# Performance work log

Hardware: AMD Instinct MI355X
Metric: run time of the kernel (lower is better)

The kernel has to match this reference:

```python
import jax, jax.numpy as jnp
import numpy as np

N_LEVELS = 16
F = 2
LOG2_T = 19
T = 1 << LOG2_T
BASE_RES = 16.0
FINEST_RES = 512.0
N_SAMPLES = 128
NEAR, FAR = 2.0, 6.0
BOX_MIN = jnp.array([-1.5, -1.5, -1.5], jnp.float32)
BOX_MAX = jnp.array([1.5, 1.5, 1.5], jnp.float32)
GEO_FEAT = 15
OUT_CH = 4

_PRIMES = np.array([1, 2654435761, 805459861], dtype=np.uint32)
_OFFSETS = np.array([[i, j, k] for i in (0, 1) for j in (0, 1) for k in (0, 1)], dtype=np.int32)  # [8,3]
_B = np.exp((np.log(FINEST_RES) - np.log(BASE_RES)) / (N_LEVELS - 1))
_RESOLUTIONS = np.floor(BASE_RES * _B ** np.arange(N_LEVELS)).astype(np.float32)


def setup_inputs() -> dict:
    key = jax.random.key(0)
    ks = jax.random.split(key, 10)
    n_rays = 16384
    o = jax.random.uniform(ks[0], (n_rays, 3), jnp.float32, -0.5, 0.5)
    d = jax.random.normal(ks[1], (n_rays, 3), jnp.float32)
    d = d / jnp.linalg.norm(d, axis=-1, keepdims=True)
    rays = jnp.concatenate([o, d], -1)
    hash_tables = jax.random.uniform(ks[2], (N_LEVELS, T, F), jnp.float32, -1e-4, 1e-4)
    def w(k, di, do):
        return jax.random.normal(k, (di, do), jnp.float32) * (1.0 / np.sqrt(di))
    return dict(
        rays=rays,
        hash_tables=hash_tables,
        ws0=w(ks[3], 32, 64), ws1=w(ks[4], 64, 64), ws2=w(ks[5], 64, 1 + GEO_FEAT),
        wc0=w(ks[6], 16 + GEO_FEAT, 64), wc1=w(ks[7], 64, 64), wc2=w(ks[8], 64, 64), wc3=w(ks[9], 64, OUT_CH - 1),
    )


def _hash_embed(x, tables):
    """Multi-res hash grid: x [P,3] world coords, tables [L,T,F] -> ([P,L*F], keep_mask [P])."""
    xc = jnp.clip(x, BOX_MIN, BOX_MAX)
    keep = jnp.all(x == xc, axis=-1)
    offs = jnp.asarray(_OFFSETS)          # [8,3]
    primes = jnp.asarray(_PRIMES)         # uint32
    feats = []
    for l in range(N_LEVELS):
        grid = (BOX_MAX - BOX_MIN) / _RESOLUTIONS[l]
        bl = jnp.floor((xc - BOX_MIN) / grid).astype(jnp.int32)   # [P,3] bottom-left voxel index
        vmin = bl.astype(jnp.float32) * grid + BOX_MIN
        wts = (xc - vmin) / grid                                  # trilinear weights [P,3]
        corners = (bl[:, None, :] + offs[None]).astype(jnp.uint32)  # [P,8,3]
        h = (corners[..., 0] * primes[0]) ^ (corners[..., 1] * primes[1]) ^ (corners[..., 2] * primes[2])
        idx = (h & jnp.uint32(T - 1)).astype(jnp.int32)           # [P,8]
        e = tables[l][idx]                                        # [P,8,F]
        w0, w1, w2 = wts[:, 0:1], wts[:, 1:2], wts[:, 2:3]
        c00 = e[:, 0] * (1 - w0) + e[:, 4] * w0
        c01 = e[:, 1] * (1 - w0) + e[:, 5] * w0
        c10 = e[:, 2] * (1 - w0) + e[:, 6] * w0
        c11 = e[:, 3] * (1 - w0) + e[:, 7] * w0
        c0 = c00 * (1 - w1) + c10 * w1
        c1 = c01 * (1 - w1) + c11 * w1
        feats.append(c0 * (1 - w2) + c1 * w2)
    return jnp.concatenate(feats, -1), keep


def _sh_encode(d):
    """Degree-4 spherical harmonics encoding, [P,3] -> [P,16]."""
    x, y, z = d[..., 0], d[..., 1], d[..., 2]
    xx, yy, zz = x * x, y * y, z * z
    xy, yz, xz = x * y, y * z, x * z
    C0 = 0.28209479177387814
    C1 = 0.4886025119029199
    C2 = (1.0925484305920792, -1.0925484305920792, 0.31539156525252005, -1.0925484305920792, 0.5462742152960396)
    C3 = (-0.5900435899266435, 2.890611442640554, -0.4570457994644658, 0.3731763325901154,
          -0.4570457994644658, 1.445305721320277, -0.5900435899266435)
    return jnp.stack([
        jnp.full_like(x, C0),
        -C1 * y, C1 * z, -C1 * x,
        C2[0] * xy, C2[1] * yz, C2[2] * (2.0 * zz - xx - yy), C2[3] * xz, C2[4] * (xx - yy),
        C3[0] * y * (3.0 * xx - yy), C3[1] * xy * z, C3[2] * y * (4.0 * zz - xx - yy),
        C3[3] * z * (2.0 * zz - 3.0 * xx - 3.0 * yy), C3[4] * x * (4.0 * zz - xx - yy),
        C3[5] * z * (xx - yy), C3[6] * x * (xx - 3.0 * yy),
    ], axis=-1)


def _forward(rays, hash_tables, ws0, ws1, ws2, wc0, wc1, wc2, wc3):
    n_rays = rays.shape[0]
    o, d = rays[:, :3], rays[:, 3:6]
    z = jnp.linspace(NEAR, FAR, N_SAMPLES, dtype=jnp.float32)
    zvals = jnp.broadcast_to(z, (n_rays, N_SAMPLES))
    pts = o[:, None, :] + d[:, None, :] * z[None, :, None]       # [N,S,3]
    P = n_rays * N_SAMPLES
    pts_f = pts.reshape(P, 3)
    dirs_f = jnp.broadcast_to(d[:, None, :], (n_rays, N_SAMPLES, 3)).reshape(P, 3)

    enc_pts, keep = _hash_embed(pts_f, hash_tables)              # [P,32], [P]
    enc_dirs = _sh_encode(dirs_f)                                # [P,16]

    # NeRFSmall: bias-free sigma net then color net
    h = jnp.maximum(enc_pts @ ws0, 0.0)
    h = jnp.maximum(h @ ws1, 0.0)
    h = h @ ws2                                                   # [P, 1+GEO_FEAT]
    sigma, geo = h[:, 0], h[:, 1:]
    hc = jnp.concatenate([enc_dirs, geo], -1)
    hc = jnp.maximum(hc @ wc0, 0.0)
    hc = jnp.maximum(hc @ wc1, 0.0)
    hc = jnp.maximum(hc @ wc2, 0.0)
    color = hc @ wc3                                              # [P, OUT_CH-1]

    sigma = jnp.where(keep, sigma, 0.0)                           # output[~keep_mask, -1] = 0
    raw = jnp.concatenate([color, sigma[:, None]], -1).reshape(n_rays, N_SAMPLES, OUT_CH)

    # Integrator (raw2outputs)
    dists = zvals[:, 1:] - zvals[:, :-1]
    dists = jnp.concatenate([dists, jnp.full((n_rays, 1), 1e10, jnp.float32)], -1)
    dists = dists * jnp.linalg.norm(d, axis=-1, keepdims=True)
    chs = jax.nn.sigmoid(raw[..., :-1])
    alpha = 1.0 - jnp.exp(-jnp.maximum(raw[..., -1], 0.0) * dists)
    trans = jnp.cumprod(1.0 - alpha + 1e-10, axis=-1)
    trans = jnp.concatenate([jnp.ones((n_rays, 1), jnp.float32), trans[:, :-1]], -1)
    weights = alpha * trans
    chs_map = jnp.einsum('ns,nsc->nc', weights, chs)
    depth_map = jnp.sum(weights * zvals, -1)
    probs = jnp.concatenate([weights, 1.0 - jnp.sum(weights, -1, keepdims=True) + 1e-6], -1)
    p = probs / jnp.sum(probs, -1, keepdims=True)
    sparsity_loss = -jnp.sum(p * jnp.log(jnp.clip(p, 1e-37)), -1)
    return chs_map, depth_map, sparsity_loss


def reference(rays, hash_tables, ws0, ws1, ws2, wc0, wc1, wc2, wc3):
    return _forward(rays, hash_tables, ws0, ws1, ws2, wc0, wc1, wc2, wc3)
```

## Files before the change

### kernel.cpp

```cpp
#include <hip/hip_runtime.h>

#define NRAYS 16384
#define NLEV  16
#define THASH 524288
#define MAXACT 48
#define MAXPTS (NRAYS*MAXACT)
#define MBLK  512
#define MGRID 1024

__device__ __forceinline__ float zval32(int i) {
  const float step = 4.0f / 127.0f;
  return __fadd_rn(2.0f, __fmul_rn((float)i, step));
}
__device__ __forceinline__ float pcoord(float o, float d, float z) {
  return __fadd_rn(o, __fmul_rn(d, z));
}

__global__ __launch_bounds__(64)
void k_classify(const float* __restrict__ rays,
                float* __restrict__ sh,
                unsigned* __restrict__ rn) {
  int r = blockIdx.x * 64 + threadIdx.x;
  if (r >= NRAYS) return;
  float ox = rays[6*r+0], oy = rays[6*r+1], oz = rays[6*r+2];
  float dx = rays[6*r+3], dy = rays[6*r+4], dz = rays[6*r+5];
  float x = dx, y = dy, z = dz;
  float xx = x*x, yy = y*y, zz = z*z, xy = x*y, yz = y*z, xz = x*z;
  float* shp = sh + 16*r;
  shp[0]  = 0.28209479177387814f;
  shp[1]  = -0.4886025119029199f * y;
  shp[2]  =  0.4886025119029199f * z;
  shp[3]  = -0.4886025119029199f * x;
  shp[4]  =  1.0925484305920792f * xy;
  shp[5]  = -1.0925484305920792f * yz;
  shp[6]  =  0.31539156525252005f * (2.0f*zz - xx - yy);
  shp[7]  = -1.0925484305920792f * xz;
  shp[8]  =  0.5462742152960396f * (xx - yy);
  shp[9]  = -0.5900435899266435f * y * (3.0f*xx - yy);
  shp[10] =  2.890611442640554f  * xy * z;
  shp[11] = -0.4570457994644658f * y * (4.0f*zz - xx - yy);
  shp[12] =  0.3731763325901154f * z * (2.0f*zz - 3.0f*xx - 3.0f*yy);
  shp[13] = -0.4570457994644658f * x * (4.0f*zz - xx - yy);
  shp[14] =  1.445305721320277f  * z * (xx - yy);
  shp[15] = -0.5900435899266435f * x * (xx - 3.0f*yy);
  int n = 0;
  for (int i = 0; i < 128; ++i) {
    float zi = zval32(i);
    float px = pcoord(ox, dx, zi);
    float py = pcoord(oy, dy, zi);
    float pz = pcoord(oz, dz, zi);
    bool in = (px >= -1.5f) && (px <= 1.5f) && (py >= -1.5f) && (py <= 1.5f)
           && (pz >= -1.5f) && (pz <= 1.5f);
    if (!in) break;
    ++n;
  }
  rn[r] = (unsigned)n;
}

__global__ __launch_bounds__(1024)
void k_scan(const unsigned* __restrict__ rn,
            unsigned* __restrict__ rbase,
            unsigned* __restrict__ counter,
            unsigned* __restrict__ plist) {
  __shared__ unsigned wsum[16];
  const int t = threadIdx.x;
  const int lane = t & 63, wid = t >> 6;
  unsigned nv[16];
  const uint4* rn4 = (const uint4*)rn;
  unsigned tot = 0;
#pragma unroll
  for (int k = 0; k < 4; ++k) {
    uint4 a = rn4[t*4 + k];
    nv[4*k+0] = a.x; nv[4*k+1] = a.y; nv[4*k+2] = a.z; nv[4*k+3] = a.w;
    tot += a.x + a.y + a.z + a.w;
  }
  unsigned incl = tot;
#pragma unroll
  for (int off = 1; off < 64; off <<= 1) {
    unsigned v = __shfl_up(incl, off);
    if (lane >= off) incl += v;
  }
  if (lane == 63) wsum[wid] = incl;
  __syncthreads();
  if (t == 0) {
    unsigned acc = 0;
#pragma unroll
    for (int w = 0; w < 16; ++w) { unsigned x = wsum[w]; wsum[w] = acc; acc += x; }
    *counter = acc;
  }
  __syncthreads();
  unsigned base = wsum[wid] + (incl - tot);
#pragma unroll
  for (int j = 0; j < 16; ++j) {
    int r = t*16 + j;
    rbase[r] = base;
    unsigned nj = nv[j];
    for (unsigned i = 0; i < nj; ++i) plist[base + i] = (unsigned)(r*128) + i;
    base += nj;
  }
}

template<int IN, int TOTOUT, int JC, bool RELU>
__device__ __forceinline__ void layer(const float* __restrict__ W, int jbase,
                                      const float* __restrict__ in,
                                      float* __restrict__ out, int lane) {
  float acc[JC];
#pragma unroll
  for (int j = 0; j < JC; ++j) acc[j] = 0.0f;
#pragma unroll 8
  for (int k = 0; k < IN; ++k) {
    float a = in[k*64 + lane];
    const float* Wk = W + k*TOTOUT + jbase;
#pragma unroll
    for (int j = 0; j < JC; ++j) acc[j] = fmaf(a, Wk[j], acc[j]);
  }
#pragma unroll
  for (int j = 0; j < JC; ++j)
    out[(jbase + j)*64 + lane] = RELU ? fmaxf(acc[j], 0.0f) : acc[j];
}

__global__ __launch_bounds__(MBLK)
void k_mlp(const float* __restrict__ rays,
           const float* __restrict__ tables,
           const float* __restrict__ w_s0, const float* __restrict__ w_s1,
           const float* __restrict__ w_s2, const float* __restrict__ w_c0,
           const float* __restrict__ w_c1, const float* __restrict__ w_c2,
           const float* __restrict__ w_c3,
           const float* __restrict__ sh,
           const unsigned* __restrict__ counter,
           const unsigned* __restrict__ plist,
           float4* __restrict__ results) {
  __shared__ float bufA[64*64];
  __shared__ float bufB[64*64];
  __shared__ float sig_s[64];
  __shared__ unsigned pid_s[64];
  const int t = threadIdx.x;
  const int lane = t & 63;
  const int q = __builtin_amdgcn_readfirstlane(t >> 6);
  {
    float pf = 0.f;
    const float4* a;
    a = (const float4*)w_s0; for (int i = t; i < 512;  i += MBLK) pf += a[i].x;
    a = (const float4*)w_s1; for (int i = t; i < 1024; i += MBLK) pf += a[i].x;
    a = (const float4*)w_s2; for (int i = t; i < 256;  i += MBLK) pf += a[i].x;
    a = (const float4*)w_c0; for (int i = t; i < 496;  i += MBLK) pf += a[i].x;
    a = (const float4*)w_c1; for (int i = t; i < 1024; i += MBLK) pf += a[i].x;
    a = (const float4*)w_c2; for (int i = t; i < 1024; i += MBLK) pf += a[i].x;
    a = (const float4*)w_c3; for (int i = t; i < 48;   i += MBLK) pf += a[i].x;
    asm volatile("" :: "v"(pf));
  }
  const unsigned count = *counter;
  const unsigned ntiles = (count + 63u) >> 6;
  const float RESF[NLEV] = {16.f,20.f,25.f,32.f,40.f,50.f,64.f,80.f,
                            101.f,128.f,161.f,203.f,256.f,322.f,406.f,512.f};
  for (unsigned tile = blockIdx.x; tile < ntiles; tile += MGRID) {
    unsigned s0 = tile << 6;
    if (t < 64) {
      unsigned s = s0 + (unsigned)t;
      pid_s[t] = (s < count) ? plist[s] : 0u;
    }
    __syncthreads();
    {
      unsigned pid = pid_s[lane];
      int r = (int)(pid >> 7);
      int i = (int)(pid & 127u);
      float zi = zval32(i);
      float px = pcoord(rays[6*r+0], rays[6*r+3], zi);
      float py = pcoord(rays[6*r+1], rays[6*r+4], zi);
      float pz = pcoord(rays[6*r+2], rays[6*r+5], zi);
      float xcx = fminf(fmaxf(px, -1.5f), 1.5f);
      float xcy = fminf(fmaxf(py, -1.5f), 1.5f);
      float xcz = fminf(fmaxf(pz, -1.5f), 1.5f);
#pragma unroll
      for (int li = 0; li < 2; ++li) {
        int l = 2*q + li;
        const float grid = 3.0f / RESF[l];
        float bfx = floorf(__fdiv_rn(__fadd_rn(xcx, 1.5f), grid));
        float bfy = floorf(__fdiv_rn(__fadd_rn(xcy, 1.5f), grid));
        float bfz = floorf(__fdiv_rn(__fadd_rn(xcz, 1.5f), grid));
        float vmx = __fadd_rn(__fmul_rn(bfx, grid), -1.5f);
        float vmy = __fadd_rn(__fmul_rn(bfy, grid), -1.5f);
        float vmz = __fadd_rn(__fmul_rn(bfz, grid), -1.5f);
        float wx = __fdiv_rn(__fsub_rn(xcx, vmx), grid);
        float wy = __fdiv_rn(__fsub_rn(xcy, vmy), grid);
        float wz = __fdiv_rn(__fsub_rn(xcz, vmz), grid);
        unsigned cx0 = (unsigned)(int)bfx, cy0 = (unsigned)(int)bfy, cz0 = (unsigned)(int)bfz;
        unsigned cx1 = cx0 + 1u, cy1 = cy0 + 1u, cz1 = cz0 + 1u;
        unsigned hy0 = cy0*2654435761u, hy1 = cy1*2654435761u;
        unsigned hz0 = cz0*805459861u,  hz1 = cz1*805459861u;
        const float2* tb = (const float2*)tables + (size_t)l*THASH;
        float2 e000 = tb[(cx0^hy0^hz0)&(THASH-1)];
        float2 e001 = tb[(cx0^hy0^hz1)&(THASH-1)];
        float2 e010 = tb[(cx0^hy1^hz0)&(THASH-1)];
        float2 e011 = tb[(cx0^hy1^hz1)&(THASH-1)];
        float2 e100 = tb[(cx1^hy0^hz0)&(THASH-1)];
        float2 e101 = tb[(cx1^hy0^hz1)&(THASH-1)];
        float2 e110 = tb[(cx1^hy1^hz0)&(THASH-1)];
        float2 e111 = tb[(cx1^hy1^hz1)&(THASH-1)];
        float iwx = 1.f-wx, iwy = 1.f-wy, iwz = 1.f-wz;
        float c00a = e000.x*iwx + e100.x*wx, c00b = e000.y*iwx + e100.y*wx;
        float c01a = e001.x*iwx + e101.x*wx, c01b = e001.y*iwx + e101.y*wx;
        float c10a = e010.x*iwx + e110.x*wx, c10b = e010.y*iwx + e110.y*wx;
        float c11a = e011.x*iwx + e111.x*wx, c11b = e011.y*iwx + e111.y*wx;
        float c0a = c00a*iwy + c10a*wy, c0b = c00b*iwy + c10b*wy;
        float c1a = c01a*iwy + c11a*wy, c1b = c01b*iwy + c11b*wy;
        bufA[(2*l+0)*64 + lane] = c0a*iwz + c1a*wz;
        bufA[(2*l+1)*64 + lane] = c0b*iwz + c1b*wz;
      }
    }
    __syncthreads();
    layer<32,64,8,true >(w_s0, q*8, bufA, bufB, lane); __syncthreads();
    layer<64,64,8,true >(w_s1, q*8, bufB, bufA, lane); __syncthreads();
    layer<64,16,2,false>(w_s2, q*2, bufA, bufB, lane); __syncthreads();
    if (q == 0) sig_s[lane] = bufB[0*64 + lane];
    for (int idx = t; idx < 31*64; idx += MBLK) {
      int k = idx >> 6, p = idx & 63;
      float v;
      if (k < 16) v = sh[(pid_s[p] >> 7)*16 + k];
      else        v = bufB[(k-15)*64 + p];
      bufA[idx] = v;
    }
    __syncthreads();
    layer<31,64,8,true >(w_c0, q*8, bufA, bufB, lane); __syncthreads();
    layer<64,64,8,true >(w_c1, q*8, bufB, bufA, lane); __syncthreads();
    layer<64,64,8,true >(w_c2, q*8, bufA, bufB, lane); __syncthreads();
    if (q < 3) layer<64,3,1,false>(w_c3, q, bufB, bufA, lane);
    __syncthreads();
    if (q == 0) {
      unsigned s = s0 + (unsigned)lane;
      if (s < count) {
        float4 res;
        res.x = sig_s[lane];
        res.y = bufA[0*64 + lane];
        res.z = bufA[1*64 + lane];
        res.w = bufA[2*64 + lane];
        results[s] = res;
      }
    }
    __syncthreads();
  }
}

__global__ __launch_bounds__(64)
void k_comp(const float* __restrict__ rays,
            const unsigned* __restrict__ rbase,
            const unsigned* __restrict__ rn,
            const float4* __restrict__ results,
            float* __restrict__ out) {
  int r = blockIdx.x * 64 + threadIdx.x;
  if (r >= NRAYS) return;
  float dx = rays[6*r+3], dy = rays[6*r+4], dz = rays[6*r+5];
  float dnorm = sqrtf(dx*dx + dy*dy + dz*dz);
  int n = (int)rn[r];
  unsigned base = rbase[r];
  const float step = 4.0f/127.0f;
  const float diststep = __fmul_rn(step, dnorm);
  float S = 0.f, ch0 = 0.f, ch1 = 0.f, ch2 = 0.f, dep = 0.f, trans = 1.f;
  for (int i = 0; i < n; ++i) {
    float4 rs = results[base + i];
    float z = zval32(i);
    float sg = fmaxf(rs.x, 0.f);
    float alpha = -expm1f(-__fmul_rn(sg, diststep));
    float w = __fmul_rn(alpha, trans);
    trans = __fmul_rn(trans, __fadd_rn(__fsub_rn(1.f, alpha), 1e-10f));
    float s0 = 1.f/(1.f + expf(-rs.y));
    float s1 = 1.f/(1.f + expf(-rs.z));
    float s2 = 1.f/(1.f + expf(-rs.w));
    S += w; ch0 += w*s0; ch1 += w*s1; ch2 += w*s2; dep += w*z;
  }
  float rem  = __fadd_rn(__fsub_rn(1.f, S), 1e-6f);
  float Stot = __fadd_rn(S, rem);
  float loss = 0.f, trans2 = 1.f;
  for (int i = 0; i < n; ++i) {
    float4 rs = results[base + i];
    float sg = fmaxf(rs.x, 0.f);
    float alpha = -expm1f(-__fmul_rn(sg, diststep));
    float w = __fmul_rn(alpha, trans2);
    trans2 = __fmul_rn(trans2, __fadd_rn(__fsub_rn(1.f, alpha), 1e-10f));
    float p = __fdiv_rn(w, Stot);
    loss += p * logf(fmaxf(p, 1e-37f));
  }
  float pl = __fdiv_rn(rem, Stot);
  loss += pl * logf(fmaxf(pl, 1e-37f));
  out[3*r+0] = ch0; out[3*r+1] = ch1; out[3*r+2] = ch2;
  out[3*NRAYS + r] = dep;
  out[4*NRAYS + r] = -loss;
}

extern "C" void kernel_launch(void* const* d_in, const int* in_sizes, int n_in,
                              void* d_out, int out_size, void* d_ws, size_t ws_size,
                              hipStream_t stream) {
  const float* rays   = (const float*)d_in[0];
  const float* tables = (const float*)d_in[1];
  const float* ws0    = (const float*)d_in[2];
  const float* ws1    = (const float*)d_in[3];
  const float* ws2    = (const float*)d_in[4];
  const float* wc0    = (const float*)d_in[5];
  const float* wc1    = (const float*)d_in[6];
  const float* wc2    = (const float*)d_in[7];
  const float* wc3    = (const float*)d_in[8];

  char* ws = (char*)d_ws;
  unsigned* counter = (unsigned*)ws;
  unsigned* rbase   = (unsigned*)(ws + 256);
  unsigned* rn      = (unsigned*)(ws + 256 + 65536);
  float*    sh      = (float*)  (ws + 256 + 131072);
  float4*   results = (float4*) (ws + 1179904);
  unsigned* plist   = (unsigned*)(ws + 1179904 + (size_t)MAXPTS*16);

  k_classify<<<NRAYS/64, 64, 0, stream>>>(rays, sh, rn);
  k_scan<<<1, 1024, 0, stream>>>(rn, rbase, counter, plist);
  k_mlp<<<MGRID, MBLK, 0, stream>>>(rays, tables, ws0, ws1, ws2,
                                    wc0, wc1, wc2, wc3, sh, counter, plist, results);
  k_comp<<<NRAYS/64, 64, 0, stream>>>(rays, rbase, rn, results, (float*)d_out);
}
```

Baseline: 216.0 us.

## Stage all MLP weights in LDS and run two tiles per 1024-thread block

The fused MLP kernel now copies every network weight into dynamic shared memory once per block and reads them from LDS with vectorized float4/float2 loads, instead of reading weights from global memory in every layer. Blocks grow to 1024 threads, each handling two 64-point tiles in parallel, on a persistent grid of 256 blocks. This is meant to cut repeated global/L2 weight traffic. In exchange the block needs about 137 KB of LDS, which limits occupancy to one block per CU, and block-wide barriers now couple the two tile groups.

New measurement: 254.3 us. +17.8%, slower.

```diff
diff --git a/kernel.cpp b/kernel.cpp
--- a/kernel.cpp
+++ b/kernel.cpp
@@ -5,8 +5,22 @@
 #define THASH 524288
 #define MAXACT 48
 #define MAXPTS (NRAYS*MAXACT)
-#define MBLK  512
-#define MGRID 1024
+#define MBLK2 1024
+#define MGRID2 256
+
+#define OFF_S0 0
+#define OFF_S1 2048
+#define OFF_S2 6144
+#define OFF_C0 7168
+#define OFF_C1 9152
+#define OFF_C2 13248
+#define OFF_C3 17344
+#define OFF_BUFA 17536
+#define OFF_BUFB 25728
+#define OFF_SIG  33920
+#define OFF_PID  34048
+#define SMEM_FLOATS 34176
+#define SMEM_BYTES  (SMEM_FLOATS*4)
 
 __device__ __forceinline__ float zval32(int i) {
   const float step = 4.0f / 127.0f;
@@ -100,26 +114,46 @@
   }
 }
 
+extern __shared__ float smem[];
+
 template<int IN, int TOTOUT, int JC, bool RELU>
-__device__ __forceinline__ void layer(const float* __restrict__ W, int jbase,
-                                      const float* __restrict__ in,
-                                      float* __restrict__ out, int lane) {
+__device__ __forceinline__ void layer_lds(const float* Wl, int jbase,
+                                          const float* in, float* out, int lane) {
   float acc[JC];
 #pragma unroll
   for (int j = 0; j < JC; ++j) acc[j] = 0.0f;
-#pragma unroll 8
-  for (int k = 0; k < IN; ++k) {
-    float a = in[k*64 + lane];
-    const float* Wk = W + k*TOTOUT + jbase;
-#pragma unroll
-    for (int j = 0; j < JC; ++j) acc[j] = fmaf(a, Wk[j], acc[j]);
+  if constexpr (JC == 8) {
+#pragma unroll 4
+    for (int k = 0; k < IN; ++k) {
+      float a = in[k*64 + lane];
+      const float4* w4 = (const float4*)(Wl + k*TOTOUT + jbase);
+      float4 wa = w4[0], wb = w4[1];
+      acc[0] = fmaf(a, wa.x, acc[0]); acc[1] = fmaf(a, wa.y, acc[1]);
+      acc[2] = fmaf(a, wa.z, acc[2]); acc[3] = fmaf(a, wa.w, acc[3]);
+      acc[4] = fmaf(a, wb.x, acc[4]); acc[5] = fmaf(a, wb.y, acc[5]);
+      acc[6] = fmaf(a, wb.z, acc[6]); acc[7] = fmaf(a, wb.w, acc[7]);
+    }
+  } else if constexpr (JC == 2) {
+#pragma unroll 4
+    for (int k = 0; k < IN; ++k) {
+      float a = in[k*64 + lane];
+      float2 w = *(const float2*)(Wl + k*TOTOUT + jbase);
+      acc[0] = fmaf(a, w.x, acc[0]); acc[1] = fmaf(a, w.y, acc[1]);
+    }
+  } else {
+#pragma unroll 4
+    for (int k = 0; k < IN; ++k) {
+      float a = in[k*64 + lane];
+#pragma unroll
+      for (int j = 0; j < JC; ++j) acc[j] = fmaf(a, Wl[k*TOTOUT + jbase + j], acc[j]);
+    }
   }
 #pragma unroll
   for (int j = 0; j < JC; ++j)
     out[(jbase + j)*64 + lane] = RELU ? fmaxf(acc[j], 0.0f) : acc[j];
 }
 
-__global__ __launch_bounds__(MBLK)
+__global__ __launch_bounds__(MBLK2)
 void k_mlp(const float* __restrict__ rays,
            const float* __restrict__ tables,
            const float* __restrict__ w_s0, const float* __restrict__ w_s1,
@@ -130,37 +164,43 @@
            const unsigned* __restrict__ counter,
            const unsigned* __restrict__ plist,
            float4* __restrict__ results) {
-  __shared__ float bufA[64*64];
-  __shared__ float bufB[64*64];
-  __shared__ float sig_s[64];
-  __shared__ unsigned pid_s[64];
   const int t = threadIdx.x;
+  {
+    float4* d = (float4*)smem;
+    const float4* s;
+    s = (const float4*)w_s0; for (int i = t; i < 512;  i += MBLK2) d[i]        = s[i];
+    s = (const float4*)w_s1; for (int i = t; i < 1024; i += MBLK2) d[512+i]    = s[i];
+    s = (const float4*)w_s2; for (int i = t; i < 256;  i += MBLK2) d[1536+i]   = s[i];
+    s = (const float4*)w_c0; for (int i = t; i < 496;  i += MBLK2) d[1792+i]   = s[i];
+    s = (const float4*)w_c1; for (int i = t; i < 1024; i += MBLK2) d[2288+i]   = s[i];
+    s = (const float4*)w_c2; for (int i = t; i < 1024; i += MBLK2) d[3312+i]   = s[i];
+    s = (const float4*)w_c3; for (int i = t; i < 48;   i += MBLK2) d[4336+i]   = s[i];
+  }
+  const int g    = t >> 9;
+  const int tg   = t & 511;
   const int lane = t & 63;
-  const int q = __builtin_amdgcn_readfirstlane(t >> 6);
-  {
-    float pf = 0.f;
-    const float4* a;
-    a = (const float4*)w_s0; for (int i = t; i < 512;  i += MBLK) pf += a[i].x;
-    a = (const float4*)w_s1; for (int i = t; i < 1024; i += MBLK) pf += a[i].x;
-    a = (const float4*)w_s2; for (int i = t; i < 256;  i += MBLK) pf += a[i].x;
-    a = (const float4*)w_c0; for (int i = t; i < 496;  i += MBLK) pf += a[i].x;
-    a = (const float4*)w_c1; for (int i = t; i < 1024; i += MBLK) pf += a[i].x;
-    a = (const float4*)w_c2; for (int i = t; i < 1024; i += MBLK) pf += a[i].x;
-    a = (const float4*)w_c3; for (int i = t; i < 48;   i += MBLK) pf += a[i].x;
-    asm volatile("" :: "v"(pf));
-  }
-  const unsigned count = *counter;
+  const int q    = __builtin_amdgcn_readfirstlane((t >> 6) & 7);
+  float*    Wl     = smem;
+  float*    bufA   = smem + OFF_BUFA + (g << 12);
+  float*    bufB   = smem + OFF_BUFB + (g << 12);
+  float*    sig_s  = smem + OFF_SIG  + g*64;
+  unsigned* pid_s  = (unsigned*)(smem + OFF_PID) + g*64;
+  __syncthreads();
+  const unsigned count  = *counter;
   const unsigned ntiles = (count + 63u) >> 6;
+  const unsigned rounds = (ntiles + 511u) >> 9;
   const float RESF[NLEV] = {16.f,20.f,25.f,32.f,40.f,50.f,64.f,80.f,
                             101.f,128.f,161.f,203.f,256.f,322.f,406.f,512.f};
-  for (unsigned tile = blockIdx.x; tile < ntiles; tile += MGRID) {
-    unsigned s0 = tile << 6;
-    if (t < 64) {
-      unsigned s = s0 + (unsigned)t;
-      pid_s[t] = (s < count) ? plist[s] : 0u;
-    }
-    __syncthreads();
-    {
+  for (unsigned rd = 0; rd < rounds; ++rd) {
+    const unsigned tile = rd*512u + (unsigned)blockIdx.x*2u + (unsigned)g;
+    const bool active = (tile < ntiles);
+    const unsigned s0 = tile << 6;
+    if (active && tg < 64) {
+      unsigned s = s0 + (unsigned)tg;
+      pid_s[tg] = (s < count) ? plist[s] : 0u;
+    }
+    __syncthreads();
+    if (active) {
       unsigned pid = pid_s[lane];
       int r = (int)(pid >> 7);
       int i = (int)(pid & 127u);
@@ -209,24 +249,32 @@
       }
     }
     __syncthreads();
-    layer<32,64,8,true >(w_s0, q*8, bufA, bufB, lane); __syncthreads();
-    layer<64,64,8,true >(w_s1, q*8, bufB, bufA, lane); __syncthreads();
-    layer<64,16,2,false>(w_s2, q*2, bufA, bufB, lane); __syncthreads();
-    if (q == 0) sig_s[lane] = bufB[0*64 + lane];
-    for (int idx = t; idx < 31*64; idx += MBLK) {
-      int k = idx >> 6, p = idx & 63;
-      float v;
-      if (k < 16) v = sh[(pid_s[p] >> 7)*16 + k];
-      else        v = bufB[(k-15)*64 + p];
-      bufA[idx] = v;
-    }
-    __syncthreads();
-    layer<31,64,8,true >(w_c0, q*8, bufA, bufB, lane); __syncthreads();
-    layer<64,64,8,true >(w_c1, q*8, bufB, bufA, lane); __syncthreads();
-    layer<64,64,8,true >(w_c2, q*8, bufA, bufB, lane); __syncthreads();
-    if (q < 3) layer<64,3,1,false>(w_c3, q, bufB, bufA, lane);
-    __syncthreads();
-    if (q == 0) {
+    if (active) layer_lds<32,64,8,true >(Wl+OFF_S0, q*8, bufA, bufB, lane);
+    __syncthreads();
+    if (active) layer_lds<64,64,8,true >(Wl+OFF_S1, q*8, bufB, bufA, lane);
+    __syncthreads();
+    if (active) layer_lds<64,16,2,false>(Wl+OFF_S2, q*2, bufA, bufB, lane);
+    __syncthreads();
+    if (active) {
+      if (q == 0) sig_s[lane] = bufB[0*64 + lane];
+      for (int idx = tg; idx < 31*64; idx += 512) {
+        int k = idx >> 6, p = idx & 63;
+        float v;
+        if (k < 16) v = sh[(pid_s[p] >> 7)*16 + k];
+        else        v = bufB[(k-15)*64 + p];
+        bufA[idx] = v;
+      }
+    }
+    __syncthreads();
+    if (active) layer_lds<31,64,8,true >(Wl+OFF_C0, q*8, bufA, bufB, lane);
+    __syncthreads();
+    if (active) layer_lds<64,64,8,true >(Wl+OFF_C1, q*8, bufB, bufA, lane);
+    __syncthreads();
+    if (active) layer_lds<64,64,8,true >(Wl+OFF_C2, q*8, bufA, bufB, lane);
+    __syncthreads();
+    if (active && q < 3) layer_lds<64,3,1,false>(Wl+OFF_C3, q, bufB, bufA, lane);
+    __syncthreads();
+    if (active && q == 0) {
       unsigned s = s0 + (unsigned)lane;
       if (s < count) {
         float4 res;
@@ -290,6 +338,12 @@
 extern "C" void kernel_launch(void* const* d_in, const int* in_sizes, int n_in,
                               void* d_out, int out_size, void* d_ws, size_t ws_size,
                               hipStream_t stream) {
+  static int smem_set = 0;
+  if (!smem_set) {
+    hipFuncSetAttribute((const void*)k_mlp,
+                        hipFuncAttributeMaxDynamicSharedMemorySize, SMEM_BYTES);
+    smem_set = 1;
+  }
   const float* rays   = (const float*)d_in[0];
   const float* tables = (const float*)d_in[1];
   const float* ws0    = (const float*)d_in[2];
@@ -310,7 +364,8 @@
 
   k_classify<<<NRAYS/64, 64, 0, stream>>>(rays, sh, rn);
   k_scan<<<1, 1024, 0, stream>>>(rn, rbase, counter, plist);
-  k_mlp<<<MGRID, MBLK, 0, stream>>>(rays, tables, ws0, ws1, ws2,
-                                    wc0, wc1, wc2, wc3, sh, counter, plist, results);
+  k_mlp<<<MGRID2, MBLK2, SMEM_BYTES, stream>>>(rays, tables, ws0, ws1, ws2,
+                                               wc0, wc1, wc2, wc3, sh, counter,
+                                               plist, results);
   k_comp<<<NRAYS/64, 64, 0, stream>>>(rays, rbase, rn, results, (float*)d_out);
 }
```

## Fuse classify, scan, MLP and compositing into one cooperative persistent kernel

Applied to the files above, without the earlier changes.

Replaces the four separate launches with a single cooperative kernel of 768 blocks of 512 threads, using grid-wide syncs between the classify, scan, MLP and compositing phases. The aim is to remove launch gaps and per-kernel ramp-up and drain between stages. The scan is still done by one block, and the MLP loop now strides by 768 blocks instead of 1024. The weight-prefetch warmup loop is dropped. The old four-kernel path stays as a fallback if the cooperative launch fails. Risks are the cost of each grid.sync, 768 blocks possibly not all being co-resident (which makes the cooperative launch fail), and the light classify and compositing phases using few threads per block.

Measured after the change: 468.7 us. 2.17x slower.

```diff
diff --git a/kernel.cpp b/kernel.cpp
--- a/kernel.cpp
+++ b/kernel.cpp
@@ -1,10 +1,14 @@
 #include <hip/hip_runtime.h>
+#include <hip/hip_cooperative_groups.h>
+
+namespace cg = cooperative_groups;
 
 #define NRAYS 16384
 #define NLEV  16
 #define THASH 524288
 #define MAXACT 48
 #define MAXPTS (NRAYS*MAXACT)
+#define FGRID 768
 #define MBLK  512
 #define MGRID 1024
 
@@ -16,12 +20,9 @@
   return __fadd_rn(o, __fmul_rn(d, z));
 }
 
-__global__ __launch_bounds__(64)
-void k_classify(const float* __restrict__ rays,
-                float* __restrict__ sh,
-                unsigned* __restrict__ rn) {
-  int r = blockIdx.x * 64 + threadIdx.x;
-  if (r >= NRAYS) return;
+__device__ __forceinline__ void classify_body(const float* __restrict__ rays,
+                                              float* __restrict__ sh,
+                                              unsigned* __restrict__ rn, int r) {
   float ox = rays[6*r+0], oy = rays[6*r+1], oz = rays[6*r+2];
   float dx = rays[6*r+3], dy = rays[6*r+4], dz = rays[6*r+5];
   float x = dx, y = dy, z = dz;
@@ -57,198 +58,11 @@
   rn[r] = (unsigned)n;
 }
 
-__global__ __launch_bounds__(1024)
-void k_scan(const unsigned* __restrict__ rn,
-            unsigned* __restrict__ rbase,
-            unsigned* __restrict__ counter,
-            unsigned* __restrict__ plist) {
-  __shared__ unsigned wsum[16];
-  const int t = threadIdx.x;
-  const int lane = t & 63, wid = t >> 6;
-  unsigned nv[16];
-  const uint4* rn4 = (const uint4*)rn;
-  unsigned tot = 0;
-#pragma unroll
-  for (int k = 0; k < 4; ++k) {
-    uint4 a = rn4[t*4 + k];
-    nv[4*k+0] = a.x; nv[4*k+1] = a.y; nv[4*k+2] = a.z; nv[4*k+3] = a.w;
-    tot += a.x + a.y + a.z + a.w;
-  }
-  unsigned incl = tot;
-#pragma unroll
-  for (int off = 1; off < 64; off <<= 1) {
-    unsigned v = __shfl_up(incl, off);
-    if (lane >= off) incl += v;
-  }
-  if (lane == 63) wsum[wid] = incl;
-  __syncthreads();
-  if (t == 0) {
-    unsigned acc = 0;
-#pragma unroll
-    for (int w = 0; w < 16; ++w) { unsigned x = wsum[w]; wsum[w] = acc; acc += x; }
-    *counter = acc;
-  }
-  __syncthreads();
-  unsigned base = wsum[wid] + (incl - tot);
-#pragma unroll
-  for (int j = 0; j < 16; ++j) {
-    int r = t*16 + j;
-    rbase[r] = base;
-    unsigned nj = nv[j];
-    for (unsigned i = 0; i < nj; ++i) plist[base + i] = (unsigned)(r*128) + i;
-    base += nj;
-  }
-}
-
-template<int IN, int TOTOUT, int JC, bool RELU>
-__device__ __forceinline__ void layer(const float* __restrict__ W, int jbase,
-                                      const float* __restrict__ in,
-                                      float* __restrict__ out, int lane) {
-  float acc[JC];
-#pragma unroll
-  for (int j = 0; j < JC; ++j) acc[j] = 0.0f;
-#pragma unroll 8
-  for (int k = 0; k < IN; ++k) {
-    float a = in[k*64 + lane];
-    const float* Wk = W + k*TOTOUT + jbase;
-#pragma unroll
-    for (int j = 0; j < JC; ++j) acc[j] = fmaf(a, Wk[j], acc[j]);
-  }
-#pragma unroll
-  for (int j = 0; j < JC; ++j)
-    out[(jbase + j)*64 + lane] = RELU ? fmaxf(acc[j], 0.0f) : acc[j];
-}
-
-__global__ __launch_bounds__(MBLK)
-void k_mlp(const float* __restrict__ rays,
-           const float* __restrict__ tables,
-           const float* __restrict__ w_s0, const float* __restrict__ w_s1,
-           const float* __restrict__ w_s2, const float* __restrict__ w_c0,
-           const float* __restrict__ w_c1, const float* __restrict__ w_c2,
-           const float* __restrict__ w_c3,
-           const float* __restrict__ sh,
-           const unsigned* __restrict__ counter,
-           const unsigned* __restrict__ plist,
-           float4* __restrict__ results) {
-  __shared__ float bufA[64*64];
-  __shared__ float bufB[64*64];
-  __shared__ float sig_s[64];
-  __shared__ unsigned pid_s[64];
-  const int t = threadIdx.x;
-  const int lane = t & 63;
-  const int q = __builtin_amdgcn_readfirstlane(t >> 6);
-  {
-    float pf = 0.f;
-    const float4* a;
-    a = (const float4*)w_s0; for (int i = t; i < 512;  i += MBLK) pf += a[i].x;
-    a = (const float4*)w_s1; for (int i = t; i < 1024; i += MBLK) pf += a[i].x;
-    a = (const float4*)w_s2; for (int i = t; i < 256;  i += MBLK) pf += a[i].x;
-    a = (const float4*)w_c0; for (int i = t; i < 496;  i += MBLK) pf += a[i].x;
-    a = (const float4*)w_c1; for (int i = t; i < 1024; i += MBLK) pf += a[i].x;
-    a = (const float4*)w_c2; for (int i = t; i < 1024; i += MBLK) pf += a[i].x;
-    a = (const float4*)w_c3; for (int i = t; i < 48;   i += MBLK) pf += a[i].x;
-    asm volatile("" :: "v"(pf));
-  }
-  const unsigned count = *counter;
-  const unsigned ntiles = (count + 63u) >> 6;
-  const float RESF[NLEV] = {16.f,20.f,25.f,32.f,40.f,50.f,64.f,80.f,
-                            101.f,128.f,161.f,203.f,256.f,322.f,406.f,512.f};
-  for (unsigned tile = blockIdx.x; tile < ntiles; tile += MGRID) {
-    unsigned s0 = tile << 6;
-    if (t < 64) {
-      unsigned s = s0 + (unsigned)t;
-      pid_s[t] = (s < count) ? plist[s] : 0u;
-    }
-    __syncthreads();
-    {
-      unsigned pid = pid_s[lane];
-      int r = (int)(pid >> 7);
-      int i = (int)(pid & 127u);
-      float zi = zval32(i);
-      float px = pcoord(rays[6*r+0], rays[6*r+3], zi);
-      float py = pcoord(rays[6*r+1], rays[6*r+4], zi);
-      float pz = pcoord(rays[6*r+2], rays[6*r+5], zi);
-      float xcx = fminf(fmaxf(px, -1.5f), 1.5f);
-      float xcy = fminf(fmaxf(py, -1.5f), 1.5f);
-      float xcz = fminf(fmaxf(pz, -1.5f), 1.5f);
-#pragma unroll
-      for (int li = 0; li < 2; ++li) {
-        int l = 2*q + li;
-        const float grid = 3.0f / RESF[l];
-        float bfx = floorf(__fdiv_rn(__fadd_rn(xcx, 1.5f), grid));
-        float bfy = floorf(__fdiv_rn(__fadd_rn(xcy, 1.5f), grid));
-        float bfz = floorf(__fdiv_rn(__fadd_rn(xcz, 1.5f), grid));
-        float vmx = __fadd_rn(__fmul_rn(bfx, grid), -1.5f);
-        float vmy = __fadd_rn(__fmul_rn(bfy, grid), -1.5f);
-        float vmz = __fadd_rn(__fmul_rn(bfz, grid), -1.5f);
-        float wx = __fdiv_rn(__fsub_rn(xcx, vmx), grid);
-        float wy = __fdiv_rn(__fsub_rn(xcy, vmy), grid);
-        float wz = __fdiv_rn(__fsub_rn(xcz, vmz), grid);
-        unsigned cx0 = (unsigned)(int)bfx, cy0 = (unsigned)(int)bfy, cz0 = (unsigned)(int)bfz;
-        unsigned cx1 = cx0 + 1u, cy1 = cy0 + 1u, cz1 = cz0 + 1u;
-        unsigned hy0 = cy0*2654435761u, hy1 = cy1*2654435761u;
-        unsigned hz0 = cz0*805459861u,  hz1 = cz1*805459861u;
-        const float2* tb = (const float2*)tables + (size_t)l*THASH;
-        float2 e000 = tb[(cx0^hy0^hz0)&(THASH-1)];
-        float2 e001 = tb[(cx0^hy0^hz1)&(THASH-1)];
-        float2 e010 = tb[(cx0^hy1^hz0)&(THASH-1)];
-        float2 e011 = tb[(cx0^hy1^hz1)&(THASH-1)];
-        float2 e100 = tb[(cx1^hy0^hz0)&(THASH-1)];
-        float2 e101 = tb[(cx1^hy0^hz1)&(THASH-1)];
-        float2 e110 = tb[(cx1^hy1^hz0)&(THASH-1)];
-        float2 e111 = tb[(cx1^hy1^hz1)&(THASH-1)];
-        float iwx = 1.f-wx, iwy = 1.f-wy, iwz = 1.f-wz;
-        float c00a = e000.x*iwx + e100.x*wx, c00b = e000.y*iwx + e100.y*wx;
-        float c01a = e001.x*iwx + e101.x*wx, c01b = e001.y*iwx + e101.y*wx;
-        float c10a = e010.x*iwx + e110.x*wx, c10b = e010.y*iwx + e110.y*wx;
-        float c11a = e011.x*iwx + e111.x*wx, c11b = e011.y*iwx + e111.y*wx;
-        float c0a = c00a*iwy + c10a*wy, c0b = c00b*iwy + c10b*wy;
-        float c1a = c01a*iwy + c11a*wy, c1b = c01b*iwy + c11b*wy;
-        bufA[(2*l+0)*64 + lane] = c0a*iwz + c1a*wz;
-        bufA[(2*l+1)*64 + lane] = c0b*iwz + c1b*wz;
-      }
-    }
-    __syncthreads();
-    layer<32,64,8,true >(w_s0, q*8, bufA, bufB, lane); __syncthreads();
-    layer<64,64,8,true >(w_s1, q*8, bufB, bufA, lane); __syncthreads();
-    layer<64,16,2,false>(w_s2, q*2, bufA, bufB, lane); __syncthreads();
-    if (q == 0) sig_s[lane] = bufB[0*64 + lane];
-    for (int idx = t; idx < 31*64; idx += MBLK) {
-      int k = idx >> 6, p = idx & 63;
-      float v;
-      if (k < 16) v = sh[(pid_s[p] >> 7)*16 + k];
-      else        v = bufB[(k-15)*64 + p];
-      bufA[idx] = v;
-    }
-    __syncthreads();
-    layer<31,64,8,true >(w_c0, q*8, bufA, bufB, lane); __syncthreads();
-    layer<64,64,8,true >(w_c1, q*8, bufB, bufA, lane); __syncthreads();
-    layer<64,64,8,true >(w_c2, q*8, bufA, bufB, lane); __syncthreads();
-    if (q < 3) layer<64,3,1,false>(w_c3, q, bufB, bufA, lane);
-    __syncthreads();
-    if (q == 0) {
-      unsigned s = s0 + (unsigned)lane;
-      if (s < count) {
-        float4 res;
-        res.x = sig_s[lane];
-        res.y = bufA[0*64 + lane];
-        res.z = bufA[1*64 + lane];
-        res.w = bufA[2*64 + lane];
-        results[s] = res;
-      }
-    }
-    __syncthreads();
-  }
-}
-
-__global__ __launch_bounds__(64)
-void k_comp(const float* __restrict__ rays,
-            const unsigned* __restrict__ rbase,
-            const unsigned* __restrict__ rn,
-            const float4* __restrict__ results,
-            float* __restrict__ out) {
-  int r = blockIdx.x * 64 + threadIdx.x;
-  if (r >= NRAYS) return;
+__device__ __forceinline__ void comp_body(const float* __restrict__ rays,
+                                          const unsigned* __restrict__ rbase,
+                                          const unsigned* __restrict__ rn,
+                                          const float4* __restrict__ results,
+                                          float* __restrict__ out, int r) {
   float dx = rays[6*r+3], dy = rays[6*r+4], dz = rays[6*r+5];
   float dnorm = sqrtf(dx*dx + dy*dy + dz*dz);
   int n = (int)rn[r];
@@ -287,6 +101,293 @@
   out[4*NRAYS + r] = -loss;
 }
 
+template<int IN, int TOTOUT, int JC, bool RELU>
+__device__ __forceinline__ void layer(const float* __restrict__ W, int jbase,
+                                      const float* __restrict__ in,
+                                      float* __restrict__ out, int lane) {
+  float acc[JC];
+#pragma unroll
+  for (int j = 0; j < JC; ++j) acc[j] = 0.0f;
+#pragma unroll 8
+  for (int k = 0; k < IN; ++k) {
+    float a = in[k*64 + lane];
+    const float* Wk = W + k*TOTOUT + jbase;
+#pragma unroll
+    for (int j = 0; j < JC; ++j) acc[j] = fmaf(a, Wk[j], acc[j]);
+  }
+#pragma unroll
+  for (int j = 0; j < JC; ++j)
+    out[(jbase + j)*64 + lane] = RELU ? fmaxf(acc[j], 0.0f) : acc[j];
+}
+
+__device__ __forceinline__ void mlp_tile(const float* __restrict__ rays,
+                                         const float* __restrict__ tables,
+                                         const float* __restrict__ w_s0,
+                                         const float* __restrict__ w_s1,
+                                         const float* __restrict__ w_s2,
+                                         const float* __restrict__ w_c0,
+                                         const float* __restrict__ w_c1,
+                                         const float* __restrict__ w_c2,
+                                         const float* __restrict__ w_c3,
+                                         const float* __restrict__ sh,
+                                         const unsigned* __restrict__ plist,
+                                         float4* __restrict__ results,
+                                         float* bufA, float* bufB, float* sig_s,
+                                         unsigned* pid_s, unsigned count,
+                                         unsigned tile, int t, int lane, int q,
+                                         const float* RESF) {
+  unsigned s0 = tile << 6;
+  if (t < 64) {
+    unsigned s = s0 + (unsigned)t;
+    pid_s[t] = (s < count) ? plist[s] : 0u;
+  }
+  __syncthreads();
+  {
+    unsigned pid = pid_s[lane];
+    int r = (int)(pid >> 7);
+    int i = (int)(pid & 127u);
+    float zi = zval32(i);
+    float px = pcoord(rays[6*r+0], rays[6*r+3], zi);
+    float py = pcoord(rays[6*r+1], rays[6*r+4], zi);
+    float pz = pcoord(rays[6*r+2], rays[6*r+5], zi);
+    float xcx = fminf(fmaxf(px, -1.5f), 1.5f);
+    float xcy = fminf(fmaxf(py, -1.5f), 1.5f);
+    float xcz = fminf(fmaxf(pz, -1.5f), 1.5f);
+#pragma unroll
+    for (int li = 0; li < 2; ++li) {
+      int l = 2*q + li;
+      const float grid = 3.0f / RESF[l];
+      float bfx = floorf(__fdiv_rn(__fadd_rn(xcx, 1.5f), grid));
+      float bfy = floorf(__fdiv_rn(__fadd_rn(xcy, 1.5f), grid));
+      float bfz = floorf(__fdiv_rn(__fadd_rn(xcz, 1.5f), grid));
+      float vmx = __fadd_rn(__fmul_rn(bfx, grid), -1.5f);
+      float vmy = __fadd_rn(__fmul_rn(bfy, grid), -1.5f);
+      float vmz = __fadd_rn(__fmul_rn(bfz, grid), -1.5f);
+      float wx = __fdiv_rn(__fsub_rn(xcx, vmx), grid);
+      float wy = __fdiv_rn(__fsub_rn(xcy, vmy), grid);
+      float wz = __fdiv_rn(__fsub_rn(xcz, vmz), grid);
+      unsigned cx0 = (unsigned)(int)bfx, cy0 = (unsigned)(int)bfy, cz0 = (unsigned)(int)bfz;
+      unsigned cx1 = cx0 + 1u, cy1 = cy0 + 1u, cz1 = cz0 + 1u;
+      unsigned hy0 = cy0*2654435761u, hy1 = cy1*2654435761u;
+      unsigned hz0 = cz0*805459861u,  hz1 = cz1*805459861u;
+      const float2* tb = (const float2*)tables + (size_t)l*THASH;
+      float2 e000 = tb[(cx0^hy0^hz0)&(THASH-1)];
+      float2 e001 = tb[(cx0^hy0^hz1)&(THASH-1)];
+      float2 e010 = tb[(cx0^hy1^hz0)&(THASH-1)];
+      float2 e011 = tb[(cx0^hy1^hz1)&(THASH-1)];
+      float2 e100 = tb[(cx1^hy0^hz0)&(THASH-1)];
+      float2 e101 = tb[(cx1^hy0^hz1)&(THASH-1)];
+      float2 e110 = tb[(cx1^hy1^hz0)&(THASH-1)];
+      float2 e111 = tb[(cx1^hy1^hz1)&(THASH-1)];
+      float iwx = 1.f-wx, iwy = 1.f-wy, iwz = 1.f-wz;
+      float c00a = e000.x*iwx + e100.x*wx, c00b = e000.y*iwx + e100.y*wx;
+      float c01a = e001.x*iwx + e101.x*wx, c01b = e001.y*iwx + e101.y*wx;
+      float c10a = e010.x*iwx + e110.x*wx, c10b = e010.y*iwx + e110.y*wx;
+      float c11a = e011.x*iwx + e111.x*wx, c11b = e011.y*iwx + e111.y*wx;
+      float c0a = c00a*iwy + c10a*wy, c0b = c00b*iwy + c10b*wy;
+      float c1a = c01a*iwy + c11a*wy, c1b = c01b*iwy + c11b*wy;
+      bufA[(2*l+0)*64 + lane] = c0a*iwz + c1a*wz;
+      bufA[(2*l+1)*64 + lane] = c0b*iwz + c1b*wz;
+    }
+  }
+  __syncthreads();
+  layer<32,64,8,true >(w_s0, q*8, bufA, bufB, lane); __syncthreads();
+  layer<64,64,8,true >(w_s1, q*8, bufB, bufA, lane); __syncthreads();
+  layer<64,16,2,false>(w_s2, q*2, bufA, bufB, lane); __syncthreads();
+  if (q == 0) sig_s[lane] = bufB[0*64 + lane];
+  for (int idx = t; idx < 31*64; idx += 512) {
+    int k = idx >> 6, p = idx & 63;
+    float v;
+    if (k < 16) v = sh[(pid_s[p] >> 7)*16 + k];
+    else        v = bufB[(k-15)*64 + p];
+    bufA[idx] = v;
+  }
+  __syncthreads();
+  layer<31,64,8,true >(w_c0, q*8, bufA, bufB, lane); __syncthreads();
+  layer<64,64,8,true >(w_c1, q*8, bufB, bufA, lane); __syncthreads();
+  layer<64,64,8,true >(w_c2, q*8, bufA, bufB, lane); __syncthreads();
+  if (q < 3) layer<64,3,1,false>(w_c3, q, bufB, bufA, lane);
+  __syncthreads();
+  if (q == 0) {
+    unsigned s = s0 + (unsigned)lane;
+    if (s < count) {
+      float4 res;
+      res.x = sig_s[lane];
+      res.y = bufA[0*64 + lane];
+      res.z = bufA[1*64 + lane];
+      res.w = bufA[2*64 + lane];
+      results[s] = res;
+    }
+  }
+  __syncthreads();
+}
+
+__global__ __launch_bounds__(512, 8)
+void k_fused(const float* __restrict__ rays, const float* __restrict__ tables,
+             const float* __restrict__ w_s0, const float* __restrict__ w_s1,
+             const float* __restrict__ w_s2, const float* __restrict__ w_c0,
+             const float* __restrict__ w_c1, const float* __restrict__ w_c2,
+             const float* __restrict__ w_c3,
+             float* __restrict__ sh, unsigned* __restrict__ counter,
+             unsigned* __restrict__ rbase, unsigned* __restrict__ rn,
+             unsigned* __restrict__ plist, float4* __restrict__ results,
+             float* __restrict__ out) {
+  __shared__ float bufA[64*64];
+  __shared__ float bufB[64*64];
+  __shared__ float sig_s[64];
+  __shared__ unsigned pid_s[64];
+  __shared__ unsigned wsum[8];
+  const int t    = threadIdx.x;
+  const int lane = t & 63;
+  const int q    = __builtin_amdgcn_readfirstlane(t >> 6);
+  cg::grid_group grid = cg::this_grid();
+
+  {
+    int r = (int)blockIdx.x * 512 + t;
+    if (r < NRAYS) classify_body(rays, sh, rn, r);
+  }
+  grid.sync();
+
+  if (blockIdx.x == 0) {
+    const uint4* rn4 = (const uint4*)rn;
+    unsigned tot = 0;
+#pragma unroll
+    for (int k = 0; k < 8; ++k) {
+      uint4 a = rn4[t*8 + k];
+      tot += a.x + a.y + a.z + a.w;
+    }
+    unsigned incl = tot;
+#pragma unroll
+    for (int off = 1; off < 64; off <<= 1) {
+      unsigned v = __shfl_up(incl, off);
+      if (lane >= off) incl += v;
+    }
+    if (lane == 63) wsum[t >> 6] = incl;
+    __syncthreads();
+    if (t == 0) {
+      unsigned acc = 0;
+#pragma unroll
+      for (int w = 0; w < 8; ++w) { unsigned x = wsum[w]; wsum[w] = acc; acc += x; }
+      *counter = acc;
+    }
+    __syncthreads();
+    unsigned base = wsum[t >> 6] + (incl - tot);
+#pragma unroll
+    for (int k = 0; k < 8; ++k) {
+      uint4 a = rn4[t*8 + k];
+      unsigned nj[4] = {a.x, a.y, a.z, a.w};
+#pragma unroll
+      for (int c = 0; c < 4; ++c) {
+        int r = t*32 + k*4 + c;
+        rbase[r] = base;
+        for (unsigned i = 0; i < nj[c]; ++i) plist[base + i] = (unsigned)(r*128) + i;
+        base += nj[c];
+      }
+    }
+  }
+  grid.sync();
+
+  {
+    const unsigned count  = *counter;
+    const unsigned ntiles = (count + 63u) >> 6;
+    const float RESF[NLEV] = {16.f,20.f,25.f,32.f,40.f,50.f,64.f,80.f,
+                              101.f,128.f,161.f,203.f,256.f,322.f,406.f,512.f};
+    for (unsigned tile = blockIdx.x; tile < ntiles; tile += (unsigned)gridDim.x)
+      mlp_tile(rays, tables, w_s0, w_s1, w_s2, w_c0, w_c1, w_c2, w_c3,
+               sh, plist, results, bufA, bufB, sig_s, pid_s, count,
+               tile, t, lane, q, RESF);
+  }
+  grid.sync();
+
+  {
+    int r = (int)blockIdx.x * 512 + t;
+    if (r < NRAYS) comp_body(rays, rbase, rn, results, out, r);
+  }
+}
+
+__global__ __launch_bounds__(64)
+void k_classify(const float* __restrict__ rays, float* __restrict__ sh,
+                unsigned* __restrict__ rn) {
+  int r = blockIdx.x * 64 + threadIdx.x;
+  if (r >= NRAYS) return;
+  classify_body(rays, sh, rn, r);
+}
+
+__global__ __launch_bounds__(1024)
+void k_scan(const unsigned* __restrict__ rn, unsigned* __restrict__ rbase,
+            unsigned* __restrict__ counter, unsigned* __restrict__ plist) {
+  __shared__ unsigned wsum[16];
+  const int t = threadIdx.x;
+  const int lane = t & 63, wid = t >> 6;
+  unsigned nv[16];
+  const uint4* rn4 = (const uint4*)rn;
+  unsigned tot = 0;
+#pragma unroll
+  for (int k = 0; k < 4; ++k) {
+    uint4 a = rn4[t*4 + k];
+    nv[4*k+0] = a.x; nv[4*k+1] = a.y; nv[4*k+2] = a.z; nv[4*k+3] = a.w;
+    tot += a.x + a.y + a.z + a.w;
+  }
+  unsigned incl = tot;
+#pragma unroll
+  for (int off = 1; off < 64; off <<= 1) {
+    unsigned v = __shfl_up(incl, off);
+    if (lane >= off) incl += v;
+  }
+  if (lane == 63) wsum[wid] = incl;
+  __syncthreads();
+  if (t == 0) {
+    unsigned acc = 0;
+#pragma unroll
+    for (int w = 0; w < 16; ++w) { unsigned x = wsum[w]; wsum[w] = acc; acc += x; }
+    *counter = acc;
+  }
+  __syncthreads();
+  unsigned base = wsum[wid] + (incl - tot);
+#pragma unroll
+  for (int j = 0; j < 16; ++j) {
+    int r = t*16 + j;
+    rbase[r] = base;
+    unsigned nj = nv[j];
+    for (unsigned i = 0; i < nj; ++i) plist[base + i] = (unsigned)(r*128) + i;
+    base += nj;
+  }
+}
+
+__global__ __launch_bounds__(MBLK)
+void k_mlp(const float* __restrict__ rays, const float* __restrict__ tables,
+           const float* __restrict__ w_s0, const float* __restrict__ w_s1,
+           const float* __restrict__ w_s2, const float* __restrict__ w_c0,
+           const float* __restrict__ w_c1, const float* __restrict__ w_c2,
+           const float* __restrict__ w_c3, const float* __restrict__ sh,
+           const unsigned* __restrict__ counter, const unsigned* __restrict__ plist,
+           float4* __restrict__ results) {
+  __shared__ float bufA[64*64];
+  __shared__ float bufB[64*64];
+  __shared__ float sig_s[64];
+  __shared__ unsigned pid_s[64];
+  const int t = threadIdx.x;
+  const int lane = t & 63;
+  const int q = __builtin_amdgcn_readfirstlane(t >> 6);
+  const unsigned count = *counter;
+  const unsigned ntiles = (count + 63u) >> 6;
+  const float RESF[NLEV] = {16.f,20.f,25.f,32.f,40.f,50.f,64.f,80.f,
+                            101.f,128.f,161.f,203.f,256.f,322.f,406.f,512.f};
+  for (unsigned tile = blockIdx.x; tile < ntiles; tile += MGRID)
+    mlp_tile(rays, tables, w_s0, w_s1, w_s2, w_c0, w_c1, w_c2, w_c3,
+             sh, plist, results, bufA, bufB, sig_s, pid_s, count,
+             tile, t, lane, q, RESF);
+}
+
+__global__ __launch_bounds__(64)
+void k_comp(const float* __restrict__ rays, const unsigned* __restrict__ rbase,
+            const unsigned* __restrict__ rn, const float4* __restrict__ results,
+            float* __restrict__ out) {
+  int r = blockIdx.x * 64 + threadIdx.x;
+  if (r >= NRAYS) return;
+  comp_body(rays, rbase, rn, results, out, r);
+}
+
 extern "C" void kernel_launch(void* const* d_in, const int* in_sizes, int n_in,
                               void* d_out, int out_size, void* d_ws, size_t ws_size,
                               hipStream_t stream) {
@@ -307,10 +408,19 @@
   float*    sh      = (float*)  (ws + 256 + 131072);
   float4*   results = (float4*) (ws + 1179904);
   unsigned* plist   = (unsigned*)(ws + 1179904 + (size_t)MAXPTS*16);
-
-  k_classify<<<NRAYS/64, 64, 0, stream>>>(rays, sh, rn);
-  k_scan<<<1, 1024, 0, stream>>>(rn, rbase, counter, plist);
-  k_mlp<<<MGRID, MBLK, 0, stream>>>(rays, tables, ws0, ws1, ws2,
-                                    wc0, wc1, wc2, wc3, sh, counter, plist, results);
-  k_comp<<<NRAYS/64, 64, 0, stream>>>(rays, rbase, rn, results, (float*)d_out);
-}
+  float*    outp    = (float*)d_out;
+
+  void* kargs[] = {(void*)&rays, (void*)&tables, (void*)&ws0, (void*)&ws1,
+                   (void*)&ws2, (void*)&wc0, (void*)&wc1, (void*)&wc2,
+                   (void*)&wc3, (void*)&sh, (void*)&counter, (void*)&rbase,
+                   (void*)&rn, (void*)&plist, (void*)&results, (void*)&outp};
+  hipError_t e = hipLaunchCooperativeKernel((void*)k_fused, dim3(FGRID), dim3(512),
+                                            kargs, 0, stream);
+  if (e != hipSuccess) {
+    k_classify<<<NRAYS/64, 64, 0, stream>>>(rays, sh, rn);
+    k_scan<<<1, 1024, 0, stream>>>(rn, rbase, counter, plist);
+    k_mlp<<<MGRID, MBLK, 0, stream>>>(rays, tables, ws0, ws1, ws2,
+                                      wc0, wc1, wc2, wc3, sh, counter, plist, results);
+    k_comp<<<NRAYS/64, 64, 0, stream>>>(rays, rbase, rn, results, outp);
+  }
+}
```
